# Kernel tuning notes

Hardware: AMD Instinct MI355X
Metric: run time of the kernel (lower is better)

Reference implementation:

```python
import jax, jax.numpy as jnp
import numpy as np

NUM_EXPERTS = 16
TOP_K = 2
FFT_LEN = 512
SEQ_LEN = 512
PRED_LEN = 720
MOE_TEMP = 1.0


def setup_inputs() -> dict:
    key = jax.random.key(0)
    ks = jax.random.split(key, 5)
    x = jax.random.normal(ks[0], (8192, SEQ_LEN), dtype=jnp.float32)
    # gating network: Linear(fft_len//2 -> num_experts)
    gw = jax.random.normal(ks[1], (NUM_EXPERTS, FFT_LEN // 2), dtype=jnp.float32) * (1.0 / np.sqrt(FFT_LEN // 2))
    gb = jnp.zeros((NUM_EXPERTS,), dtype=jnp.float32)
    # experts: RLinear = instance-norm (RevIN) + Linear(seq->pred), stacked
    ew = jax.random.normal(ks[2], (NUM_EXPERTS, SEQ_LEN, PRED_LEN), dtype=jnp.float32) * (1.0 / np.sqrt(SEQ_LEN))
    eb = jnp.zeros((NUM_EXPERTS, PRED_LEN), dtype=jnp.float32)
    return {"x": x, "gw": gw, "gb": gb, "ew": ew, "eb": eb}


def periodogram(x, n):
    # x: [B, L] -> normalized power spectrum [B, n//2]
    x0 = x - jnp.mean(x, axis=1, keepdims=True)
    dft = jnp.fft.fft(x0, n=n, axis=1) / jnp.sqrt(jnp.asarray(n, x.dtype))
    I = jnp.abs(dft[:, : n // 2]) ** 2
    s = jnp.sum(I, axis=1, keepdims=True)
    s = jnp.where(s == 0, 1.0, s)
    return I / s


def expert_apply(x, ew, eb):
    # RLinear: instance normalize, linear map, de-normalize
    mu = jnp.mean(x, axis=1, keepdims=True)
    sd = jnp.std(x, axis=1, keepdims=True) + 1e-5
    xn = (x - mu) / sd  # [B, L]
    # all experts densely: [B,L] x [E,L,P] -> [E,B,P]
    y = jnp.einsum('bl,elp->ebp', xn, ew) + eb[:, None, :]
    return y * sd[None] + mu[None]  # [E, B, P]


def reference(x, gw, gb, ew, eb):
    I = periodogram(x, FFT_LEN)  # [B, n//2]
    gate = (I @ gw.T + gb) / MOE_TEMP  # eval mode: divide by temp, no noise
    topk_vals, topk_idx = jax.lax.top_k(gate, TOP_K)  # [B, k]
    gates = jax.nn.softmax(topk_vals, axis=1)  # [B, k]
    expert_out = expert_apply(x, ew, eb)  # [E, B, P]
    # gather selected experts: [B, k, P]
    sel = jnp.take_along_axis(
        jnp.transpose(expert_out, (1, 0, 2)), topk_idx[:, :, None], axis=1
    )
    return jnp.sum(gates[:, :, None] * sel, axis=1)  # [B, P]
```

## Files before the change

kernel.cpp:

```cpp
#include <hip/hip_runtime.h>
#include <hip/hip_bf16.h>
#include <math.h>

#define NEXP  16
#define SEQ   512
#define PRED  720
#define NROWS 8192
#define NFREQ 256

typedef __bf16 bf16x8 __attribute__((ext_vector_type(8)));
typedef float  f32x16 __attribute__((ext_vector_type(16)));

__device__ __forceinline__ void gload_lds16(const void* g, void* l) {
    __builtin_amdgcn_global_load_lds(
        (const __attribute__((address_space(1))) unsigned int*)g,
        (__attribute__((address_space(3))) unsigned int*)l, 16, 0, 0);
}

__device__ __forceinline__ int xcd_swizzle(int bid, int nwg) {
    const int q = nwg >> 3, r = nwg & 7;
    const int xcd = bid & 7, off = bid >> 3;
    return (xcd < r ? xcd * (q + 1) : r * (q + 1) + (xcd - r) * q) + off;
}

__global__ __launch_bounds__(256) void k_transpose_ew(const float* __restrict__ ew,
                                                      __hip_bfloat16* __restrict__ ewt)
{
    __shared__ float tile[32][33];
    const int e  = blockIdx.z;
    const int p0 = blockIdx.x * 32;
    const int l0 = blockIdx.y * 32;
    const int tx = threadIdx.x & 31;
    const int ty = threadIdx.x >> 5;
    const float* src = ew + (size_t)e * SEQ * PRED;
#pragma unroll
    for (int i = 0; i < 4; ++i) {
        int l = l0 + ty + i * 8;
        int p = p0 + tx;
        tile[ty + i * 8][tx] = (p < PRED) ? src[(size_t)l * PRED + p] : 0.f;
    }
    __syncthreads();
    __hip_bfloat16* dst = ewt + (size_t)e * PRED * SEQ;
#pragma unroll
    for (int i = 0; i < 4; ++i) {
        int p = p0 + ty + i * 8;
        int l = l0 + tx;
        if (p < PRED) dst[(size_t)p * SEQ + l] = __float2bfloat16(tile[tx][ty + i * 8]);
    }
}

__global__ __launch_bounds__(256) void k_build_dft(__hip_bfloat16* __restrict__ bthi,
                                                   __hip_bfloat16* __restrict__ btlo,
                                                   int* __restrict__ nredo)
{
    if (blockIdx.x == 0 && threadIdx.x == 0) *nredo = 0;

    const int tid  = blockIdx.x * 256 + threadIdx.x;
    const int f    = tid >> 9;
    const int lidx = tid & 511;
    const int m    = (f * lidx) & 511;

    constexpr double Cj[9] = {0.9999247018391445033, 0.9996988186962042201,
                              0.9987954562051723927, 0.9951847266721968862,
                              0.9807852804032304491, 0.9238795325112867561,
                              0.7071067811865475244, 0.0, -1.0};
    constexpr double Sj[9] = {0.0122715382857199261, 0.0245412285229122880,
                              0.0490676743274180143, 0.0980171403295606020,
                              0.1950903220161282678, 0.3826834323650897717,
                              0.7071067811865475244, 1.0, 0.0};
    double cr = 1.0, ci = 0.0;
#pragma unroll
    for (int j = 0; j < 9; ++j) {
        const bool on = (m >> j) & 1;
        const double mr = on ? Cj[j] : 1.0;
        const double mi = on ? Sj[j] : 0.0;
        const double nr = cr * mr - ci * mi;
        ci = cr * mi + ci * mr;
        cr = nr;
    }

    const size_t c0 = (size_t)(2 * f) * 512 + lidx;
    const size_t c1 = (size_t)(2 * f + 1) * 512 + lidx;
    {
        __hip_bfloat16 h = __float2bfloat16((float)cr);
        float hif = __bfloat162float(h);
        bthi[c0] = h;
        btlo[c0] = __float2bfloat16((float)(cr - (double)hif));
    }
    {
        __hip_bfloat16 h = __float2bfloat16((float)ci);
        float hif = __bfloat162float(h);
        bthi[c1] = h;
        btlo[c1] = __float2bfloat16((float)(ci - (double)hif));
    }
}

__global__ __launch_bounds__(256) void k_stats(const float* __restrict__ x,
                                               __hip_bfloat16* __restrict__ xn,
                                               __hip_bfloat16* __restrict__ xnlo,
                                               float* __restrict__ meta)
{
    const int t  = threadIdx.x;
    const int wv = t >> 6, l = t & 63;
    const int b  = blockIdx.x * 4 + wv;
    const float* xr = x + (size_t)b * SEQ;

    const float4 v0 = *(const float4*)(xr + l * 8);
    const float4 v1 = *(const float4*)(xr + l * 8 + 4);
    const double d0 = v0.x, d1 = v0.y, d2 = v0.z, d3 = v0.w;
    const double d4 = v1.x, d5 = v1.y, d6 = v1.z, d7 = v1.w;

    double s1 = ((d0 + d1) + (d2 + d3)) + ((d4 + d5) + (d6 + d7));
    double s2 = ((d0 * d0 + d1 * d1) + (d2 * d2 + d3 * d3)) +
                ((d4 * d4 + d5 * d5) + (d6 * d6 + d7 * d7));
#pragma unroll
    for (int off = 1; off < 64; off <<= 1) {
        s1 += __shfl_xor(s1, off);
        s2 += __shfl_xor(s2, off);
    }
    const double mu = s1 * (1.0 / 512.0);
    double var = s2 * (1.0 / 512.0) - mu * mu;
    if (var < 0.0) var = 0.0;
    const double sd = sqrt(var) + 1e-5, inv = 1.0 / sd;

    unsigned int hw[4], lw[4];
#define CONV(j, dj)                                                         \
    {                                                                       \
        double xnd = (dj - mu) * inv;                                       \
        __hip_bfloat16 h = __float2bfloat16((float)xnd);                    \
        float hif = __bfloat162float(h);                                    \
        __hip_bfloat16 lo = __float2bfloat16((float)(xnd - (double)hif));   \
        unsigned int hb = *(unsigned short*)&h;                             \
        unsigned int lb = *(unsigned short*)&lo;                            \
        if ((j & 1) == 0) { hw[j >> 1] = hb; lw[j >> 1] = lb; }             \
        else { hw[j >> 1] |= hb << 16; lw[j >> 1] |= lb << 16; }            \
    }
    CONV(0, d0) CONV(1, d1) CONV(2, d2) CONV(3, d3)
    CONV(4, d4) CONV(5, d5) CONV(6, d6) CONV(7, d7)
#undef CONV
    *(uint4*)(xn   + (size_t)b * SEQ + l * 8) = uint4{hw[0], hw[1], hw[2], hw[3]};
    *(uint4*)(xnlo + (size_t)b * SEQ + l * 8) = uint4{lw[0], lw[1], lw[2], lw[3]};

    if (l == 0) {
        meta[b * 4 + 0] = (float)mu;
        meta[b * 4 + 3] = (float)sd;
    }
}

__global__ __launch_bounds__(256, 3) void k_dft_gemm(
    const __hip_bfloat16* __restrict__ xn, const __hip_bfloat16* __restrict__ xnlo,
    const __hip_bfloat16* __restrict__ bthi, const __hip_bfloat16* __restrict__ btlo,
    float* __restrict__ Iout)
{
    const int wgid = xcd_swizzle(blockIdx.x, 1024);
    const int rt = wgid >> 3;
    const int ct = wgid & 7;

    __shared__ __align__(16) __hip_bfloat16 As[3][64][64];
    __shared__ __align__(16) __hip_bfloat16 Bs[3][64][64];

    const int t  = threadIdx.x;
    const int wv = t >> 6, l = t & 63;

    size_t aoff[2], boff[2];
    int ldsrow[2], ldschk[2];
#pragma unroll
    for (int i = 0; i < 2; ++i) {
        const int idx = i * 256 + t;
        const int row = idx >> 3, chk = idx & 7;
        const int swz = (row & 7) ^ ((row & 8) >> 1);
        ldsrow[i] = row; ldschk[i] = chk;
        aoff[i] = (size_t)(rt * 64 + row) * SEQ + (size_t)(chk ^ swz) * 8;
        boff[i] = (size_t)(ct * 64 + row) * SEQ + (size_t)(chk ^ swz) * 8;
    }

#define DSTAGE(buf, kk) do {                                                   \
    const int pass_ = (kk) >> 3;                                               \
    const int koff_ = ((kk) & 7) * 64;                                         \
    const __hip_bfloat16* ap_ = (pass_ == 1) ? xnlo : xn;                      \
    const __hip_bfloat16* bp_ = (pass_ == 2) ? btlo : bthi;                    \
    _Pragma("unroll")                                                          \
    for (int i_ = 0; i_ < 2; ++i_)                                             \
        gload_lds16(ap_ + aoff[i_] + koff_, &As[buf][ldsrow[i_]][ldschk[i_] * 8]); \
    _Pragma("unroll")                                                          \
    for (int i_ = 0; i_ < 2; ++i_)                                             \
        gload_lds16(bp_ + boff[i_] + koff_, &Bs[buf][ldsrow[i_]][ldschk[i_] * 8]); \
} while (0)

    f32x16 acc;
#pragma unroll
    for (int q = 0; q < 16; ++q) acc[q] = 0.f;

    const int wr = wv >> 1, wc = wv & 1;
    const int fl = l & 31, fh = l >> 5;
    const int rswz = (fl & 7) ^ ((fl & 8) >> 1);

    DSTAGE(0, 0);
    DSTAGE(1, 1);
#pragma unroll
    for (int kt = 0; kt < 24; ++kt) {
        const int cur = kt % 3;
        if (kt < 23) asm volatile("s_waitcnt vmcnt(4)" ::: "memory");
        else         asm volatile("s_waitcnt vmcnt(0)" ::: "memory");
        __builtin_amdgcn_sched_barrier(0);
        __builtin_amdgcn_s_barrier();
        __builtin_amdgcn_sched_barrier(0);
#pragma unroll
        for (int ks = 0; ks < 4; ++ks) {
            const int cc = ((ks * 2 + fh) ^ rswz) * 8;
            const bf16x8 a = *(const bf16x8*)&As[cur][wr * 32 + fl][cc];
            const bf16x8 b = *(const bf16x8*)&Bs[cur][wc * 32 + fl][cc];
            acc = __builtin_amdgcn_mfma_f32_32x32x16_bf16(a, b, acc, 0, 0, 0);
        }
        if (kt + 2 < 24) DSTAGE((kt + 2) % 3, kt + 2);
    }
#undef DSTAGE

    const int crow_base = 4 * fh;
    const int col = ct * 64 + wc * 32 + fl;
#pragma unroll
    for (int q = 0; q < 16; ++q) {
        const float v = acc[q];
        const float w = __shfl_xor(v, 1);
        if ((fl & 1) == 0) {
            const int rl = wr * 32 + (q & 3) + 8 * (q >> 2) + crow_base;
            Iout[(size_t)(rt * 64 + rl) * NFREQ + (col >> 1)] = v * v + w * w;
        }
    }
}

__global__ __launch_bounds__(256) void k_gatefin(const float* __restrict__ Iout,
                                                 const float* __restrict__ gw,
                                                 const float* __restrict__ gb,
                                                 float* __restrict__ meta,
                                                 int* __restrict__ eidx,
                                                 int* __restrict__ redo,
                                                 int* __restrict__ nredo)
{
    __shared__ float gws[NEXP * 257];
    __shared__ float Pw[4][256];
    __shared__ float Gs[4][16];

    const int t  = threadIdx.x;
    const int wv = t >> 6, l = t & 63;
    const int b  = blockIdx.x * 4 + wv;

    for (int i = t; i < NEXP * NFREQ; i += 256)
        gws[(i >> 8) * 257 + (i & 255)] = gw[i];
    __syncthreads();

    const float* Ir = Iout + (size_t)b * NFREQ;
    const float i0 = Ir[l], i1 = Ir[64 + l], i2 = Ir[128 + l], i3 = Ir[192 + l];
    Pw[wv][l] = i0; Pw[wv][64 + l] = i1; Pw[wv][128 + l] = i2; Pw[wv][192 + l] = i3;
    float ps = (i0 + i1) + (i2 + i3);
#pragma unroll
    for (int off = 1; off < 64; off <<= 1) ps += __shfl_xor(ps, off);

    const int e = l >> 2, kb = l & 3;
    float acc = 0.f;
#pragma unroll 8
    for (int j = 0; j < 64; ++j) {
        const int k = kb + 4 * j;
        acc += Pw[wv][k] * gws[e * 257 + k];
    }
    acc += __shfl_xor(acc, 1);
    acc += __shfl_xor(acc, 2);
    if (kb == 0) Gs[wv][e] = acc;

    if (l == 0) {
        const float sdiv  = (ps == 0.f) ? 1.f : ps;
        const float inv_s = 1.f / sdiv;
        float b1 = -1e30f, b2 = -1e30f, b3 = -1e30f;
        int i1b = 0, i2b = 0;
#pragma unroll
        for (int i = 0; i < NEXP; ++i) {
            float v = Gs[wv][i] * inv_s + gb[i];
            if (v > b1)      { b3 = b2; b2 = b1; i2b = i1b; b1 = v; i1b = i; }
            else if (v > b2) { b3 = b2; b2 = v; i2b = i; }
            else if (v > b3) { b3 = v; }
        }
        if (b2 - b3 < 1e-4f * fmaxf(1.f, fabsf(b1))) {
            const int r = atomicAdd(nredo, 1);
            redo[r] = b;
        } else {
            const float sd = meta[b * 4 + 3];
            const float ee = __expf(b2 - b1);
            const float w0 = 1.f / (1.f + ee);
            const float w1 = ee / (1.f + ee);
            meta[b * 4 + 1] = w0 * sd;
            meta[b * 4 + 2] = w1 * sd;
            eidx[b * 2 + 0] = i1b;
            eidx[b * 2 + 1] = i2b;
        }
    }
}

__global__ __launch_bounds__(256, 4) void k_gate64(const float* __restrict__ x,
                                                   const float* __restrict__ gw,
                                                   const float* __restrict__ gb,
                                                   float* __restrict__ meta,
                                                   int* __restrict__ eidx,
                                                   const int* __restrict__ redo,
                                                   const int* __restrict__ nredo)
{
    __shared__ double Pw[4][256];
    __shared__ double Gs[4][16];

    const int t  = threadIdx.x;
    const int wv = t >> 6, l = t & 63;
    const int n  = *nredo;

    for (int it = blockIdx.x * 4 + wv; it < n; it += gridDim.x * 4) {
        const int b = redo[it];
        const float* xr = x + (size_t)b * SEQ;

        double s1 = 0.0, s2 = 0.0;
#define DLOADV(n_) double vr##n_ = (double)xr[64 * n_ + l]; s1 += vr##n_; s2 += vr##n_ * vr##n_;
        DLOADV(0) DLOADV(1) DLOADV(2) DLOADV(3) DLOADV(4) DLOADV(5) DLOADV(6) DLOADV(7)
#undef DLOADV
        double vi0, vi1, vi2, vi3, vi4, vi5, vi6, vi7;

#pragma unroll
        for (int off = 1; off < 64; off <<= 1) {
            s1 += __shfl_xor(s1, off);
            s2 += __shfl_xor(s2, off);
        }
        const double mu = s1 * (1.0 / 512.0);
        double var = s2 * (1.0 / 512.0) - mu * mu;
        if (var < 0.0) var = 0.0;
        const double sd = sqrt(var) + 1e-5;

#define DSUB(n_) vr##n_ -= mu;
        DSUB(0) DSUB(1) DSUB(2) DSUB(3) DSUB(4) DSUB(5) DSUB(6) DSUB(7)
#undef DSUB

        {
            const double C = 0.70710678118654752440084436210485;
            double a0 = vr0 + vr4, a1 = vr1 + vr5, a2 = vr2 + vr6, a3 = vr3 + vr7;
            double d0 = vr0 - vr4, d1 = vr1 - vr5, d2 = vr2 - vr6, d3 = vr3 - vr7;
            double c0 = a0 + a2, c2 = a0 - a2, c1 = a1 + a3;
            double c3i = a3 - a1;
            double e1r = C * (d1 - d3), e1i = -C * (d1 + d3);
            vr0 = c0 + c1;   vi0 = 0.0;
            vr1 = c0 - c1;   vi1 = 0.0;
            vr2 = c2;        vi2 = c3i;
            vr3 = c2;        vi3 = -c3i;
            vr4 = d0 + e1r;  vi4 = -d2 + e1i;
            vr5 = d0 - e1r;  vi5 = -d2 - e1i;
            vr6 = d0 - e1r;  vi6 =  d2 + e1i;
            vr7 = d0 + e1r;  vi7 =  d2 - e1i;
        }

        double w1r = 1.0, w1i = 0.0;
        {
            constexpr double Cr[6] = {0.9999247018391445033, 0.9996988186962042201,
                                      0.9987954562051723927, 0.9951847266721968862,
                                      0.9807852804032304491, 0.9238795325112867561};
            constexpr double Ci[6] = {-0.0122715382857199261, -0.0245412285229122880,
                                      -0.0490676743274180143, -0.0980171403295606020,
                                      -0.1950903220161282678, -0.3826834323650897717};
#pragma unroll
            for (int j = 0; j < 6; ++j) {
                const bool on = (l >> j) & 1;
                const double mr = on ? Cr[j] : 1.0;
                const double mi = on ? Ci[j] : 0.0;
                const double nr = w1r * mr - w1i * mi;
                w1i = w1r * mi + w1i * mr;
                w1r = nr;
            }
        }

        {
            double wkr = w1r, wki = w1i;
#define DTWID(n_) { double tr_ = vr##n_ * wkr - vi##n_ * wki; \
                    vi##n_ = vr##n_ * wki + vi##n_ * wkr; vr##n_ = tr_; }
#define DWSTEP() { double nr_ = wkr * w1r - wki * w1i; \
                   wki = wkr * w1i + wki * w1r; wkr = nr_; }
            DTWID(4) DWSTEP() DTWID(2) DWSTEP() DTWID(6) DWSTEP() DTWID(1)
            DWSTEP() DTWID(5) DWSTEP() DTWID(3) DWSTEP() DTWID(7)
#undef DTWID
#undef DWSTEP
        }

        double twr, twi;
        {
            double w2r = w1r * w1r - w1i * w1i, w2i = 2.0 * w1r * w1i;
            double w4r = w2r * w2r - w2i * w2i, w4i = 2.0 * w2r * w2i;
            twr = w4r * w4r - w4i * w4i; twi = 2.0 * w4r * w4i;
        }
#define DBF(R, I, h, hi, ter, tei) { \
        double br_ = __shfl_xor(R, h); double bi_ = __shfl_xor(I, h); \
        double dr_ = hi ? (R - br_) : (R + br_); \
        double di_ = hi ? (I - bi_) : (I + bi_); \
        R = dr_ * ter - di_ * tei; I = dr_ * tei + di_ * ter; }
#define DSTG(hc) { \
        const bool hi_ = (l & hc) != 0; \
        const double ter_ = hi_ ? twr : 1.0; \
        const double tei_ = hi_ ? twi : 0.0; \
        DBF(vr0, vi0, hc, hi_, ter_, tei_) DBF(vr1, vi1, hc, hi_, ter_, tei_) \
        DBF(vr2, vi2, hc, hi_, ter_, tei_) DBF(vr3, vi3, hc, hi_, ter_, tei_) \
        DBF(vr4, vi4, hc, hi_, ter_, tei_) DBF(vr5, vi5, hc, hi_, ter_, tei_) \
        DBF(vr6, vi6, hc, hi_, ter_, tei_) DBF(vr7, vi7, hc, hi_, ter_, tei_) \
        double ntr_ = twr * twr - twi * twi; twi = 2.0 * twr * twi; twr = ntr_; }
        DSTG(32) DSTG(16) DSTG(8) DSTG(4) DSTG(2) DSTG(1)
#undef DSTG
#undef DBF

        const int k2 = (int)(__brev((unsigned)l) >> 26);
        double ps = 0.0;
        if ((l & 1) == 0) {
            const int kb = 8 * k2;
            double P;
            P = vr0 * vr0 + vi0 * vi0; ps += P; Pw[wv][0 + kb] = P;
            P = vr1 * vr1 + vi1 * vi1; ps += P; Pw[wv][4 + kb] = P;
            P = vr2 * vr2 + vi2 * vi2; ps += P; Pw[wv][2 + kb] = P;
            P = vr3 * vr3 + vi3 * vi3; ps += P; Pw[wv][6 + kb] = P;
            P = vr4 * vr4 + vi4 * vi4; ps += P; Pw[wv][1 + kb] = P;
            P = vr5 * vr5 + vi5 * vi5; ps += P; Pw[wv][5 + kb] = P;
            P = vr6 * vr6 + vi6 * vi6; ps += P; Pw[wv][3 + kb] = P;
            P = vr7 * vr7 + vi7 * vi7; ps += P; Pw[wv][7 + kb] = P;
        }
#pragma unroll
        for (int off = 1; off < 64; off <<= 1) ps += __shfl_xor(ps, off);

        {
            const int e = l >> 2, kb = l & 3;
            double acc = 0.0;
#pragma unroll 8
            for (int j = 0; j < 64; ++j) {
                int k = kb + 4 * j;
                acc += Pw[wv][k] * (double)gw[e * NFREQ + k];
            }
            acc += __shfl_xor(acc, 1);
            acc += __shfl_xor(acc, 2);
            if (kb == 0) Gs[wv][e] = acc;
        }

        if (l == 0) {
            const double sdiv  = (ps == 0.0) ? 1.0 : ps;
            const double inv_s = 1.0 / sdiv;
            double best = -1e300, best2 = -1e300;
            int i0b = 0, i1b = 0;
#pragma unroll
            for (int i = 0; i < NEXP; ++i) {
                double v = Gs[wv][i] * inv_s + (double)gb[i];
                if (v > best)       { best2 = best; i1b = i0b; best = v; i0b = i; }
                else if (v > best2) { best2 = v; i1b = i; }
            }
            const double eexp = (double)__expf((float)(best2 - best));
            const double w0 = 1.0 / (1.0 + eexp);
            const double w1 = eexp / (1.0 + eexp);
            meta[b * 4 + 0] = (float)mu;
            meta[b * 4 + 1] = (float)(w0 * sd);
            meta[b * 4 + 2] = (float)(w1 * sd);
            meta[b * 4 + 3] = (float)sd;
            eidx[b * 2 + 0] = i0b;
            eidx[b * 2 + 1] = i1b;
        }
    }
}

__global__ __launch_bounds__(256) void k_count(const int* __restrict__ eidx,
                                               int* __restrict__ blockHist)
{
    __shared__ int h[32];
    const int t   = threadIdx.x;
    const int blk = blockIdx.x;
    if (t < 32) h[t] = 0;
    __syncthreads();
    const int b  = blk * 256 + t;
    const int e0 = eidx[2 * b];
    const int e1 = eidx[2 * b + 1];
    atomicAdd(&h[e0], 1);
    atomicAdd(&h[16 + e1], 1);
    __syncthreads();
    if (t < 32) blockHist[(t >> 4) * 512 + blk * 16 + (t & 15)] = h[t];
}

__global__ void k_scan(const int* __restrict__ blockHist, int* __restrict__ counts,
                       int* __restrict__ offs, int* __restrict__ toff,
                       int* __restrict__ base)
{
    __shared__ int cnt[32];
    __shared__ int off_s[32];
    const int j = threadIdx.x;
    if (j < 32) {
        const int s = j >> 4, e = j & 15;
        int acc = 0;
        for (int blk = 0; blk < 32; ++blk) acc += blockHist[s * 512 + blk * 16 + e];
        cnt[j] = acc;
        counts[j] = acc;
    }
    __syncthreads();
    if (j < 2) {
        int acc = 0, tac = 0;
        for (int i = 0; i < NEXP; ++i) {
            const int c = cnt[j * 16 + i];
            off_s[j * 16 + i] = acc;
            offs[j * 16 + i]  = acc;
            acc += c;
            toff[j * 17 + i] = tac;
            tac += (c + 63) >> 6;
        }
        toff[j * 17 + 16] = tac;
    }
    __syncthreads();
    if (j < 32) {
        const int s = j >> 4, e = j & 15;
        int run = off_s[j];
        for (int blk = 0; blk < 32; ++blk) {
            base[s * 512 + blk * 16 + e] = run;
            run += blockHist[s * 512 + blk * 16 + e];
        }
    }
}

__global__ __launch_bounds__(256) void k_scatter(const int* __restrict__ eidx,
                                                 const int* __restrict__ base,
                                                 int* __restrict__ lists)
{
    __shared__ int whist[2][4][16];
    const int t   = threadIdx.x;
    const int wv  = t >> 6, l = t & 63;
    const int blk = blockIdx.x;
    const int b   = blk * 256 + t;
    const int e0  = eidx[2 * b];
    const int e1  = eidx[2 * b + 1];
    const unsigned long long before = (1ULL << l) - 1ULL;

    unsigned long long m0 = 0, m1 = 0;
#pragma unroll
    for (int bb = 0; bb < 16; ++bb) {
        unsigned long long m = __ballot(e0 == bb);
        if (e0 == bb) m0 = m;
        if (l == 0) whist[0][wv][bb] = __popcll(m);
    }
#pragma unroll
    for (int bb = 0; bb < 16; ++bb) {
        unsigned long long m = __ballot(e1 == bb);
        if (e1 == bb) m1 = m;
        if (l == 0) whist[1][wv][bb] = __popcll(m);
    }
    __syncthreads();

    int p0 = __popcll(m0 & before);
    int p1 = __popcll(m1 & before);
    for (int w = 0; w < 4; ++w) {
        if (w < wv) {
            p0 += whist[0][w][e0];
            p1 += whist[1][w][e1];
        }
    }
    lists[base[blk * 16 + e0] + p0]                 = b;
    lists[NROWS + base[512 + blk * 16 + e1] + p1]   = b;
}

template <int SLOT>
__global__ __launch_bounds__(256, 3) void k_expert_gemm(
    const __hip_bfloat16* __restrict__ xn, const __hip_bfloat16* __restrict__ ewt,
    const float* __restrict__ eb, const float* __restrict__ meta,
    const int* __restrict__ lists, const int* __restrict__ offs,
    const int* __restrict__ counts, const int* __restrict__ toff,
    float* __restrict__ out)
{
    const int wgid = xcd_swizzle(blockIdx.x, 1728);
    const int tid  = wgid / 12;
    const int ct   = wgid % 12;
    if (tid >= toff[SLOT * 17 + 16]) return;
    int e = 0;
#pragma unroll
    for (int i = 0; i < 15; ++i) e += (toff[SLOT * 17 + e + 1] <= tid) ? 1 : 0;
    const int rt  = tid - toff[SLOT * 17 + e];
    const int n_e = counts[SLOT * NEXP + e];

    __shared__ __align__(16) __hip_bfloat16 As[3][64][64];
    __shared__ __align__(16) __hip_bfloat16 Bs[3][64][64];
    __shared__ int   rowB[64];
    __shared__ float rowMu[64];
    __shared__ float rowC[64];

    const int t  = threadIdx.x;
    const int wv = t >> 6, l = t & 63;
    const int* list = lists + SLOT * NROWS + offs[SLOT * NEXP + e];
    if (t < 64) {
        int r  = rt * 64 + t;
        int bb = (r < n_e) ? list[r] : -1;
        rowB[t]  = bb;
        rowMu[t] = (bb >= 0) ? meta[bb * 4] : 0.f;
        rowC[t]  = (bb >= 0) ? meta[bb * 4 + 1 + SLOT] : 0.f;
    }
    __syncthreads();

    const __hip_bfloat16* asrc[2];
    const __hip_bfloat16* bsrc[2];
    int ldsrow[2], ldschk[2];
#pragma unroll
    for (int i = 0; i < 2; ++i) {
        const int idx = i * 256 + t;
        const int row = idx >> 3, chk = idx & 7;
        const int swz = (row & 7) ^ ((row & 8) >> 1);
        ldsrow[i] = row; ldschk[i] = chk;
        const int ab  = rowB[row];
        asrc[i] = xn + ((ab >= 0) ? (size_t)ab * SEQ : 0) + (size_t)(chk ^ swz) * 8;
        const int gc  = ct * 64 + row;
        const int gcc = (gc < PRED) ? gc : (PRED - 1);
        bsrc[i] = ewt + ((size_t)e * PRED + gcc) * SEQ + (size_t)(chk ^ swz) * 8;
    }

#define STAGE(buf, koff) do {                                                      \
    _Pragma("unroll")                                                              \
    for (int i_ = 0; i_ < 2; ++i_)                                                 \
        gload_lds16(asrc[i_] + (koff), &As[buf][ldsrow[i_]][ldschk[i_] * 8]);      \
    _Pragma("unroll")                                                              \
    for (int i_ = 0; i_ < 2; ++i_)                                                 \
        gload_lds16(bsrc[i_] + (koff), &Bs[buf][ldsrow[i_]][ldschk[i_] * 8]);      \
} while (0)

    f32x16 acc;
#pragma unroll
    for (int q = 0; q < 16; ++q) acc[q] = 0.f;

    const int wr = wv >> 1, wc = wv & 1;
    const int fl = l & 31, fh = l >> 5;
    const int rswz = (fl & 7) ^ ((fl & 8) >> 1);

    STAGE(0, 0);
    STAGE(1, 64);
#pragma unroll
    for (int kt = 0; kt < 8; ++kt) {
        const int cur = kt % 3;
        if (kt < 7) asm volatile("s_waitcnt vmcnt(4)" ::: "memory");
        else        asm volatile("s_waitcnt vmcnt(0)" ::: "memory");
        __builtin_amdgcn_sched_barrier(0);
        __builtin_amdgcn_s_barrier();
        __builtin_amdgcn_sched_barrier(0);
#pragma unroll
        for (int ks = 0; ks < 4; ++ks) {
            const int cc = ((ks * 2 + fh) ^ rswz) * 8;
            const bf16x8 a = *(const bf16x8*)&As[cur][wr * 32 + fl][cc];
            const bf16x8 b = *(const bf16x8*)&Bs[cur][wc * 32 + fl][cc];
            acc = __builtin_amdgcn_mfma_f32_32x32x16_bf16(a, b, acc, 0, 0, 0);
        }
        if (kt + 2 < 8) STAGE((kt + 2) % 3, (kt + 2) * 64);
    }
#undef STAGE

    const int crow_base = 4 * fh;
    const int col = ct * 64 + wc * 32 + fl;
    const bool cok = (col < PRED);
    const float ebv = cok ? eb[e * PRED + col] : 0.f;
#pragma unroll
    for (int q = 0; q < 16; ++q) {
        const int rl = wr * 32 + (q & 3) + 8 * (q >> 2) + crow_base;
        const int bb = rowB[rl];
        if (!cok || bb < 0) continue;
        const float v = acc[q] + ebv;
        float* op = out + (size_t)bb * PRED + col;
        if (SLOT == 0) *op = rowMu[rl] + rowC[rl] * v;
        else           *op += rowC[rl] * v;
    }
}

extern "C" void kernel_launch(void* const* d_in, const int* in_sizes, int n_in,
                              void* d_out, int out_size, void* d_ws, size_t ws_size,
                              hipStream_t stream)
{
    const float* x  = (const float*)d_in[0];
    const float* gw = (const float*)d_in[1];
    const float* gb = (const float*)d_in[2];
    const float* ew = (const float*)d_in[3];
    const float* eb = (const float*)d_in[4];
    float* out = (float*)d_out;
    char*  ws  = (char*)d_ws;

    constexpr size_t XN_OFF   = 0;
    constexpr size_t XN_SZ    = (size_t)NROWS * SEQ * 2;
    constexpr size_t XNLO_OFF = XN_OFF + XN_SZ;
    constexpr size_t EWT_OFF  = XNLO_OFF + XN_SZ;
    constexpr size_t EWT_SZ   = (size_t)NEXP * PRED * SEQ * 2;
    constexpr size_t BTHI_OFF = EWT_OFF + EWT_SZ;
    constexpr size_t BT_SZ    = (size_t)512 * 512 * 2;
    constexpr size_t BTLO_OFF = BTHI_OFF + BT_SZ;
    constexpr size_t IOUT_OFF = BTLO_OFF + BT_SZ;
    constexpr size_t IOUT_SZ  = (size_t)NROWS * NFREQ * 4;
    constexpr size_t META_OFF = IOUT_OFF + IOUT_SZ;
    constexpr size_t META_SZ  = (size_t)NROWS * 4 * 4;
    constexpr size_t EIDX_OFF = META_OFF + META_SZ;
    constexpr size_t EIDX_SZ  = (size_t)NROWS * 2 * 4;
    constexpr size_t LIST_OFF = EIDX_OFF + EIDX_SZ;
    constexpr size_t LIST_SZ  = (size_t)2 * NROWS * 4;
    constexpr size_t CNT_OFF  = LIST_OFF + LIST_SZ;
    constexpr size_t OFFS_OFF = CNT_OFF + 144;
    constexpr size_t TOFF_OFF = OFFS_OFF + 128;
    constexpr size_t BH_OFF   = TOFF_OFF + 160;
    constexpr size_t BASE_OFF = BH_OFF + 4096;
    constexpr size_t REDO_OFF = BASE_OFF + 4096;

    __hip_bfloat16* xn   = (__hip_bfloat16*)(ws + XN_OFF);
    __hip_bfloat16* xnlo = (__hip_bfloat16*)(ws + XNLO_OFF);
    __hip_bfloat16* ewt  = (__hip_bfloat16*)(ws + EWT_OFF);
    __hip_bfloat16* bthi = (__hip_bfloat16*)(ws + BTHI_OFF);
    __hip_bfloat16* btlo = (__hip_bfloat16*)(ws + BTLO_OFF);
    float* Iout  = (float*)(ws + IOUT_OFF);
    float* meta  = (float*)(ws + META_OFF);
    int* eidx    = (int*)(ws + EIDX_OFF);
    int* lists   = (int*)(ws + LIST_OFF);
    int* counts  = (int*)(ws + CNT_OFF);
    int* nredo   = (int*)(ws + CNT_OFF + 128);
    int* offs    = (int*)(ws + OFFS_OFF);
    int* toff    = (int*)(ws + TOFF_OFF);
    int* bhist   = (int*)(ws + BH_OFF);
    int* base    = (int*)(ws + BASE_OFF);
    int* redo    = (int*)(ws + REDO_OFF);

    k_build_dft<<<dim3(512), dim3(256), 0, stream>>>(bthi, btlo, nredo);
    k_transpose_ew<<<dim3(23, 16, NEXP), dim3(256), 0, stream>>>(ew, ewt);
    k_stats<<<dim3(NROWS / 4), dim3(256), 0, stream>>>(x, xn, xnlo, meta);
    k_dft_gemm<<<dim3(1024), dim3(256), 0, stream>>>(xn, xnlo, bthi, btlo, Iout);
    k_gatefin<<<dim3(NROWS / 4), dim3(256), 0, stream>>>(Iout, gw, gb, meta, eidx,
                                                         redo, nredo);
    k_gate64<<<dim3(64), dim3(256), 0, stream>>>(x, gw, gb, meta, eidx, redo, nredo);
    k_count<<<dim3(32), dim3(256), 0, stream>>>(eidx, bhist);
    k_scan<<<dim3(1), dim3(64), 0, stream>>>(bhist, counts, offs, toff, base);
    k_scatter<<<dim3(32), dim3(256), 0, stream>>>(eidx, base, lists);
    k_expert_gemm<0><<<dim3(1728), dim3(256), 0, stream>>>(
        xn, ewt, eb, meta, lists, offs, counts, toff, out);
    k_expert_gemm<1><<<dim3(1728), dim3(256), 0, stream>>>(
        xn, ewt, eb, meta, lists, offs, counts, toff, out);
}
```

Baseline: 150.5 us.

## Merge preprocessing kernels and run both expert slots in one launch

Folds the DFT-basis build, expert-weight transpose and row-stats kernels into a single launch that dispatches on block ID. The two per-slot expert GEMM launches become one grid covering both slots. A precomputed tile descriptor table replaces the per-block expert search, and slot 1 writes to a separate buffer. A new merge kernel then adds that buffer into the output, which removes launch gaps and lets both slots overlap at the cost of an extra read-modify-write pass over the output.

Result: faster. 141.7 us (-5.9%).

```diff
diff --git a/kernel.cpp b/kernel.cpp
--- a/kernel.cpp
+++ b/kernel.cpp
@@ -23,127 +23,133 @@
     return (xcd < r ? xcd * (q + 1) : r * (q + 1) + (xcd - r) * q) + off;
 }
 
-__global__ __launch_bounds__(256) void k_transpose_ew(const float* __restrict__ ew,
-                                                      __hip_bfloat16* __restrict__ ewt)
-{
-    __shared__ float tile[32][33];
-    const int e  = blockIdx.z;
-    const int p0 = blockIdx.x * 32;
-    const int l0 = blockIdx.y * 32;
-    const int tx = threadIdx.x & 31;
-    const int ty = threadIdx.x >> 5;
-    const float* src = ew + (size_t)e * SEQ * PRED;
-#pragma unroll
-    for (int i = 0; i < 4; ++i) {
-        int l = l0 + ty + i * 8;
-        int p = p0 + tx;
-        tile[ty + i * 8][tx] = (p < PRED) ? src[(size_t)l * PRED + p] : 0.f;
-    }
-    __syncthreads();
-    __hip_bfloat16* dst = ewt + (size_t)e * PRED * SEQ;
-#pragma unroll
-    for (int i = 0; i < 4; ++i) {
-        int p = p0 + ty + i * 8;
-        int l = l0 + tx;
-        if (p < PRED) dst[(size_t)p * SEQ + l] = __float2bfloat16(tile[tx][ty + i * 8]);
-    }
-}
-
-__global__ __launch_bounds__(256) void k_build_dft(__hip_bfloat16* __restrict__ bthi,
-                                                   __hip_bfloat16* __restrict__ btlo,
-                                                   int* __restrict__ nredo)
-{
-    if (blockIdx.x == 0 && threadIdx.x == 0) *nredo = 0;
-
-    const int tid  = blockIdx.x * 256 + threadIdx.x;
-    const int f    = tid >> 9;
-    const int lidx = tid & 511;
-    const int m    = (f * lidx) & 511;
-
-    constexpr double Cj[9] = {0.9999247018391445033, 0.9996988186962042201,
-                              0.9987954562051723927, 0.9951847266721968862,
-                              0.9807852804032304491, 0.9238795325112867561,
-                              0.7071067811865475244, 0.0, -1.0};
-    constexpr double Sj[9] = {0.0122715382857199261, 0.0245412285229122880,
-                              0.0490676743274180143, 0.0980171403295606020,
-                              0.1950903220161282678, 0.3826834323650897717,
-                              0.7071067811865475244, 1.0, 0.0};
-    double cr = 1.0, ci = 0.0;
-#pragma unroll
-    for (int j = 0; j < 9; ++j) {
-        const bool on = (m >> j) & 1;
-        const double mr = on ? Cj[j] : 1.0;
-        const double mi = on ? Sj[j] : 0.0;
-        const double nr = cr * mr - ci * mi;
-        ci = cr * mi + ci * mr;
-        cr = nr;
-    }
-
-    const size_t c0 = (size_t)(2 * f) * 512 + lidx;
-    const size_t c1 = (size_t)(2 * f + 1) * 512 + lidx;
+__global__ __launch_bounds__(256) void k_preproc(const float* __restrict__ ew,
+                                                 const float* __restrict__ x,
+                                                 __hip_bfloat16* __restrict__ ewt,
+                                                 __hip_bfloat16* __restrict__ bthi,
+                                                 __hip_bfloat16* __restrict__ btlo,
+                                                 __hip_bfloat16* __restrict__ xn,
+                                                 __hip_bfloat16* __restrict__ xnlo,
+                                                 float* __restrict__ meta,
+                                                 int* __restrict__ nredo)
+{
+    const int bid = blockIdx.x;
+    const int t   = threadIdx.x;
+
+    if (bid < 512) {
+        if (bid == 0 && t == 0) *nredo = 0;
+        const int tid  = bid * 256 + t;
+        const int f    = tid >> 9;
+        const int lidx = tid & 511;
+        const int m    = (f * lidx) & 511;
+
+        constexpr double Cj[9] = {0.9999247018391445033, 0.9996988186962042201,
+                                  0.9987954562051723927, 0.9951847266721968862,
+                                  0.9807852804032304491, 0.9238795325112867561,
+                                  0.7071067811865475244, 0.0, -1.0};
+        constexpr double Sj[9] = {0.0122715382857199261, 0.0245412285229122880,
+                                  0.0490676743274180143, 0.0980171403295606020,
+                                  0.1950903220161282678, 0.3826834323650897717,
+                                  0.7071067811865475244, 1.0, 0.0};
+        double cr = 1.0, ci = 0.0;
+#pragma unroll
+        for (int j = 0; j < 9; ++j) {
+            const bool on = (m >> j) & 1;
+            const double mr = on ? Cj[j] : 1.0;
+            const double mi = on ? Sj[j] : 0.0;
+            const double nr = cr * mr - ci * mi;
+            ci = cr * mi + ci * mr;
+            cr = nr;
+        }
+        const size_t c0 = (size_t)(2 * f) * 512 + lidx;
+        const size_t c1 = (size_t)(2 * f + 1) * 512 + lidx;
+        {
+            __hip_bfloat16 h = __float2bfloat16((float)cr);
+            float hif = __bfloat162float(h);
+            bthi[c0] = h;
+            btlo[c0] = __float2bfloat16((float)(cr - (double)hif));
+        }
+        {
+            __hip_bfloat16 h = __float2bfloat16((float)ci);
+            float hif = __bfloat162float(h);
+            bthi[c1] = h;
+            btlo[c1] = __float2bfloat16((float)(ci - (double)hif));
+        }
+        return;
+    }
+
+    if (bid < 6400) {
+        __shared__ float tile[32][33];
+        const int rel = bid - 512;
+        const int e   = rel / 368;
+        const int rem = rel % 368;
+        const int p0  = (rem % 23) * 32;
+        const int l0  = (rem / 23) * 32;
+        const int tx  = t & 31;
+        const int ty  = t >> 5;
+        const float* src = ew + (size_t)e * SEQ * PRED;
+#pragma unroll
+        for (int i = 0; i < 4; ++i) {
+            int l = l0 + ty + i * 8;
+            int p = p0 + tx;
+            tile[ty + i * 8][tx] = (p < PRED) ? src[(size_t)l * PRED + p] : 0.f;
+        }
+        __syncthreads();
+        __hip_bfloat16* dst = ewt + (size_t)e * PRED * SEQ;
+#pragma unroll
+        for (int i = 0; i < 4; ++i) {
+            int p = p0 + ty + i * 8;
+            int l = l0 + tx;
+            if (p < PRED) dst[(size_t)p * SEQ + l] = __float2bfloat16(tile[tx][ty + i * 8]);
+        }
+        return;
+    }
+
     {
-        __hip_bfloat16 h = __float2bfloat16((float)cr);
-        float hif = __bfloat162float(h);
-        bthi[c0] = h;
-        btlo[c0] = __float2bfloat16((float)(cr - (double)hif));
-    }
-    {
-        __hip_bfloat16 h = __float2bfloat16((float)ci);
-        float hif = __bfloat162float(h);
-        bthi[c1] = h;
-        btlo[c1] = __float2bfloat16((float)(ci - (double)hif));
-    }
-}
-
-__global__ __launch_bounds__(256) void k_stats(const float* __restrict__ x,
-                                               __hip_bfloat16* __restrict__ xn,
-                                               __hip_bfloat16* __restrict__ xnlo,
-                                               float* __restrict__ meta)
-{
-    const int t  = threadIdx.x;
-    const int wv = t >> 6, l = t & 63;
-    const int b  = blockIdx.x * 4 + wv;
-    const float* xr = x + (size_t)b * SEQ;
-
-    const float4 v0 = *(const float4*)(xr + l * 8);
-    const float4 v1 = *(const float4*)(xr + l * 8 + 4);
-    const double d0 = v0.x, d1 = v0.y, d2 = v0.z, d3 = v0.w;
-    const double d4 = v1.x, d5 = v1.y, d6 = v1.z, d7 = v1.w;
-
-    double s1 = ((d0 + d1) + (d2 + d3)) + ((d4 + d5) + (d6 + d7));
-    double s2 = ((d0 * d0 + d1 * d1) + (d2 * d2 + d3 * d3)) +
-                ((d4 * d4 + d5 * d5) + (d6 * d6 + d7 * d7));
-#pragma unroll
-    for (int off = 1; off < 64; off <<= 1) {
-        s1 += __shfl_xor(s1, off);
-        s2 += __shfl_xor(s2, off);
-    }
-    const double mu = s1 * (1.0 / 512.0);
-    double var = s2 * (1.0 / 512.0) - mu * mu;
-    if (var < 0.0) var = 0.0;
-    const double sd = sqrt(var) + 1e-5, inv = 1.0 / sd;
-
-    unsigned int hw[4], lw[4];
+        const int wv = t >> 6, l = t & 63;
+        const int b  = (bid - 6400) * 4 + wv;
+        const float* xr = x + (size_t)b * SEQ;
+
+        const float4 v0 = *(const float4*)(xr + l * 8);
+        const float4 v1 = *(const float4*)(xr + l * 8 + 4);
+        const double d0 = v0.x, d1 = v0.y, d2 = v0.z, d3 = v0.w;
+        const double d4 = v1.x, d5 = v1.y, d6 = v1.z, d7 = v1.w;
+
+        double s1 = ((d0 + d1) + (d2 + d3)) + ((d4 + d5) + (d6 + d7));
+        double s2 = ((d0 * d0 + d1 * d1) + (d2 * d2 + d3 * d3)) +
+                    ((d4 * d4 + d5 * d5) + (d6 * d6 + d7 * d7));
+#pragma unroll
+        for (int off = 1; off < 64; off <<= 1) {
+            s1 += __shfl_xor(s1, off);
+            s2 += __shfl_xor(s2, off);
+        }
+        const double mu = s1 * (1.0 / 512.0);
+        double var = s2 * (1.0 / 512.0) - mu * mu;
+        if (var < 0.0) var = 0.0;
+        const double sd = sqrt(var) + 1e-5, inv = 1.0 / sd;
+
+        unsigned int hw[4], lw[4];
 #define CONV(j, dj)                                                         \
-    {                                                                       \
-        double xnd = (dj - mu) * inv;                                       \
-        __hip_bfloat16 h = __float2bfloat16((float)xnd);                    \
-        float hif = __bfloat162float(h);                                    \
-        __hip_bfloat16 lo = __float2bfloat16((float)(xnd - (double)hif));   \
-        unsigned int hb = *(unsigned short*)&h;                             \
-        unsigned int lb = *(unsigned short*)&lo;                            \
-        if ((j & 1) == 0) { hw[j >> 1] = hb; lw[j >> 1] = lb; }             \
-        else { hw[j >> 1] |= hb << 16; lw[j >> 1] |= lb << 16; }            \
-    }
-    CONV(0, d0) CONV(1, d1) CONV(2, d2) CONV(3, d3)
-    CONV(4, d4) CONV(5, d5) CONV(6, d6) CONV(7, d7)
+        {                                                                   \
+            double xnd = (dj - mu) * inv;                                   \
+            __hip_bfloat16 h = __float2bfloat16((float)xnd);                \
+            float hif = __bfloat162float(h);                                \
+            __hip_bfloat16 lo = __float2bfloat16((float)(xnd - (double)hif)); \
+            unsigned int hb = *(unsigned short*)&h;                         \
+            unsigned int lb = *(unsigned short*)&lo;                        \
+            if ((j & 1) == 0) { hw[j >> 1] = hb; lw[j >> 1] = lb; }         \
+            else { hw[j >> 1] |= hb << 16; lw[j >> 1] |= lb << 16; }        \
+        }
+        CONV(0, d0) CONV(1, d1) CONV(2, d2) CONV(3, d3)
+        CONV(4, d4) CONV(5, d5) CONV(6, d6) CONV(7, d7)
 #undef CONV
-    *(uint4*)(xn   + (size_t)b * SEQ + l * 8) = uint4{hw[0], hw[1], hw[2], hw[3]};
-    *(uint4*)(xnlo + (size_t)b * SEQ + l * 8) = uint4{lw[0], lw[1], lw[2], lw[3]};
-
-    if (l == 0) {
-        meta[b * 4 + 0] = (float)mu;
-        meta[b * 4 + 3] = (float)sd;
+        *(uint4*)(xn   + (size_t)b * SEQ + l * 8) = uint4{hw[0], hw[1], hw[2], hw[3]};
+        *(uint4*)(xnlo + (size_t)b * SEQ + l * 8) = uint4{lw[0], lw[1], lw[2], lw[3]};
+
+        if (l == 0) {
+            meta[b * 4 + 0] = (float)mu;
+            meta[b * 4 + 3] = (float)sd;
+        }
     }
 }
 
@@ -478,7 +484,7 @@
 }
 
 __global__ void k_scan(const int* __restrict__ blockHist, int* __restrict__ counts,
-                       int* __restrict__ offs, int* __restrict__ toff,
+                       int* __restrict__ offs, int* __restrict__ tdesc,
                        int* __restrict__ base)
 {
     __shared__ int cnt[32];
@@ -493,16 +499,16 @@
     }
     __syncthreads();
     if (j < 2) {
-        int acc = 0, tac = 0;
+        int acc = 0, tt = 0;
         for (int i = 0; i < NEXP; ++i) {
             const int c = cnt[j * 16 + i];
             off_s[j * 16 + i] = acc;
             offs[j * 16 + i]  = acc;
             acc += c;
-            toff[j * 17 + i] = tac;
-            tac += (c + 63) >> 6;
-        }
-        toff[j * 17 + 16] = tac;
+            const int nt = (c + 63) >> 6;
+            for (int k = 0; k < nt; ++k) tdesc[j * 160 + tt++] = (i << 16) | k;
+        }
+        for (; tt < 160; ++tt) tdesc[j * 160 + tt] = -1;
     }
     __syncthreads();
     if (j < 32) {
@@ -555,23 +561,23 @@
     lists[NROWS + base[512 + blk * 16 + e1] + p1]   = b;
 }
 
-template <int SLOT>
 __global__ __launch_bounds__(256, 3) void k_expert_gemm(
     const __hip_bfloat16* __restrict__ xn, const __hip_bfloat16* __restrict__ ewt,
     const float* __restrict__ eb, const float* __restrict__ meta,
     const int* __restrict__ lists, const int* __restrict__ offs,
-    const int* __restrict__ counts, const int* __restrict__ toff,
-    float* __restrict__ out)
-{
-    const int wgid = xcd_swizzle(blockIdx.x, 1728);
-    const int tid  = wgid / 12;
-    const int ct   = wgid % 12;
-    if (tid >= toff[SLOT * 17 + 16]) return;
-    int e = 0;
-#pragma unroll
-    for (int i = 0; i < 15; ++i) e += (toff[SLOT * 17 + e + 1] <= tid) ? 1 : 0;
-    const int rt  = tid - toff[SLOT * 17 + e];
-    const int n_e = counts[SLOT * NEXP + e];
+    const int* __restrict__ counts, const int* __restrict__ tdesc,
+    float* __restrict__ out, float* __restrict__ out2)
+{
+    const int wgid = xcd_swizzle(blockIdx.x, 3456);
+    const int slot = wgid / 1728;
+    const int rem  = wgid - slot * 1728;
+    const int tid  = rem / 12;
+    const int ct   = rem % 12;
+    const int d    = tdesc[slot * 160 + tid];
+    if (d < 0) return;
+    const int e  = d >> 16;
+    const int rt = d & 0xffff;
+    const int n_e = counts[slot * NEXP + e];
 
     __shared__ __align__(16) __hip_bfloat16 As[3][64][64];
     __shared__ __align__(16) __hip_bfloat16 Bs[3][64][64];
@@ -581,13 +587,13 @@
 
     const int t  = threadIdx.x;
     const int wv = t >> 6, l = t & 63;
-    const int* list = lists + SLOT * NROWS + offs[SLOT * NEXP + e];
+    const int* list = lists + slot * NROWS + offs[slot * NEXP + e];
     if (t < 64) {
         int r  = rt * 64 + t;
         int bb = (r < n_e) ? list[r] : -1;
         rowB[t]  = bb;
         rowMu[t] = (bb >= 0) ? meta[bb * 4] : 0.f;
-        rowC[t]  = (bb >= 0) ? meta[bb * 4 + 1 + SLOT] : 0.f;
+        rowC[t]  = (bb >= 0) ? meta[bb * 4 + 1 + slot] : 0.f;
     }
     __syncthreads();
 
@@ -655,10 +661,19 @@
         const int bb = rowB[rl];
         if (!cok || bb < 0) continue;
         const float v = acc[q] + ebv;
-        float* op = out + (size_t)bb * PRED + col;
-        if (SLOT == 0) *op = rowMu[rl] + rowC[rl] * v;
-        else           *op += rowC[rl] * v;
-    }
+        if (slot == 0) out [(size_t)bb * PRED + col] = rowMu[rl] + rowC[rl] * v;
+        else           out2[(size_t)bb * PRED + col] = rowC[rl] * v;
+    }
+}
+
+__global__ __launch_bounds__(256) void k_merge(float* __restrict__ out,
+                                               const float* __restrict__ out2)
+{
+    const int i = blockIdx.x * 256 + threadIdx.x;
+    float4 a = ((float4*)out)[i];
+    const float4 b = ((const float4*)out2)[i];
+    a.x += b.x; a.y += b.y; a.z += b.z; a.w += b.w;
+    ((float4*)out)[i] = a;
 }
 
 extern "C" void kernel_launch(void* const* d_in, const int* in_sizes, int n_in,
@@ -691,10 +706,11 @@
     constexpr size_t LIST_SZ  = (size_t)2 * NROWS * 4;
     constexpr size_t CNT_OFF  = LIST_OFF + LIST_SZ;
     constexpr size_t OFFS_OFF = CNT_OFF + 144;
-    constexpr size_t TOFF_OFF = OFFS_OFF + 128;
-    constexpr size_t BH_OFF   = TOFF_OFF + 160;
+    constexpr size_t TDSC_OFF = OFFS_OFF + 128;
+    constexpr size_t BH_OFF   = TDSC_OFF + 1280;
     constexpr size_t BASE_OFF = BH_OFF + 4096;
     constexpr size_t REDO_OFF = BASE_OFF + 4096;
+    constexpr size_t OUT2_OFF = REDO_OFF + (size_t)NROWS * 4;
 
     __hip_bfloat16* xn   = (__hip_bfloat16*)(ws + XN_OFF);
     __hip_bfloat16* xnlo = (__hip_bfloat16*)(ws + XNLO_OFF);
@@ -708,23 +724,22 @@
     int* counts  = (int*)(ws + CNT_OFF);
     int* nredo   = (int*)(ws + CNT_OFF + 128);
     int* offs    = (int*)(ws + OFFS_OFF);
-    int* toff    = (int*)(ws + TOFF_OFF);
+    int* tdesc   = (int*)(ws + TDSC_OFF);
     int* bhist   = (int*)(ws + BH_OFF);
     int* base    = (int*)(ws + BASE_OFF);
     int* redo    = (int*)(ws + REDO_OFF);
-
-    k_build_dft<<<dim3(512), dim3(256), 0, stream>>>(bthi, btlo, nredo);
-    k_transpose_ew<<<dim3(23, 16, NEXP), dim3(256), 0, stream>>>(ew, ewt);
-    k_stats<<<dim3(NROWS / 4), dim3(256), 0, stream>>>(x, xn, xnlo, meta);
+    float* out2  = (float*)(ws + OUT2_OFF);
+
+    k_preproc<<<dim3(8448), dim3(256), 0, stream>>>(ew, x, ewt, bthi, btlo,
+                                                    xn, xnlo, meta, nredo);
     k_dft_gemm<<<dim3(1024), dim3(256), 0, stream>>>(xn, xnlo, bthi, btlo, Iout);
     k_gatefin<<<dim3(NROWS / 4), dim3(256), 0, stream>>>(Iout, gw, gb, meta, eidx,
                                                          redo, nredo);
     k_gate64<<<dim3(64), dim3(256), 0, stream>>>(x, gw, gb, meta, eidx, redo, nredo);
     k_count<<<dim3(32), dim3(256), 0, stream>>>(eidx, bhist);
-    k_scan<<<dim3(1), dim3(64), 0, stream>>>(bhist, counts, offs, toff, base);
+    k_scan<<<dim3(1), dim3(64), 0, stream>>>(bhist, counts, offs, tdesc, base);
     k_scatter<<<dim3(32), dim3(256), 0, stream>>>(eidx, base, lists);
-    k_expert_gemm<0><<<dim3(1728), dim3(256), 0, stream>>>(
-        xn, ewt, eb, meta, lists, offs, counts, toff, out);
-    k_expert_gemm<1><<<dim3(1728), dim3(256), 0, stream>>>(
-        xn, ewt, eb, meta, lists, offs, counts, toff, out);
-}
+    k_expert_gemm<<<dim3(3456), dim3(256), 0, stream>>>(
+        xn, ewt, eb, meta, lists, offs, counts, tdesc, out, out2);
+    k_merge<<<dim3(NROWS * PRED / 1024), dim3(256), 0, stream>>>(out, out2);
+}
```
